# Kernel tuning notes

Measured on AMD Instinct MI355X. Metric: run time of the kernel, lower is better.

## Reference

```python
import jax, jax.numpy as jnp
import numpy as np

VOCAB, E, H, L = 32000, 512, 1024, 2
B, T = 64, 256


def _lstm_layer(x_seq, Wx, Wh, b):
    """x_seq: [T, B, in]. Gate order i,f,n,o stacked along last dim of Wx/Wh/b."""
    Bsz = x_seq.shape[1]
    h0 = jnp.zeros((Bsz, H), x_seq.dtype)
    c0 = jnp.zeros((Bsz, H), x_seq.dtype)

    def step(carry, x_t):
        h, c = carry
        g = x_t @ Wx + h @ Wh + b  # [B, 4H]
        i_t, f_t, n_t, o_t = jnp.split(g, 4, axis=-1)
        i_t = jax.nn.sigmoid(i_t)
        f_t = jax.nn.sigmoid(f_t)
        n_t = jnp.tanh(n_t)
        o_t = jax.nn.sigmoid(o_t)
        c_new = f_t * c + i_t * n_t
        h_new = o_t * jnp.tanh(c_new)
        return (h_new, c_new), h_new

    (h_n, c_n), ys = jax.lax.scan(step, (h0, c0), x_seq)
    return ys, h_n, c_n


def setup_inputs() -> dict:
    key = jax.random.key(0)
    ks = jax.random.split(key, 8)
    src = jax.random.randint(ks[0], (B, T), 0, VOCAB, dtype=jnp.int64 if jax.config.jax_enable_x64 else jnp.int32)
    lengths = jnp.sort(jax.random.randint(ks[1], (B,), T // 2, T + 1, dtype=jnp.int32))[::-1]
    lengths = lengths.at[0].set(T)  # guarantee max length == T (pad_packed_sequence output width)
    s = 0.05
    return {
        "src": src,
        "src_lengths": lengths,
        "embedding": jax.random.normal(ks[2], (VOCAB, E), jnp.float32) * s,
        "Wx0": jax.random.normal(ks[3], (E, 4 * H), jnp.float32) * s,
        "Wh0": jax.random.normal(ks[4], (H, 4 * H), jnp.float32) * s,
        "b0": jnp.zeros((4 * H,), jnp.float32),
        "Wx1": jax.random.normal(ks[5], (H, 4 * H), jnp.float32) * s,
        "Wh1": jax.random.normal(ks[6], (H, 4 * H), jnp.float32) * s,
        "b1": jnp.zeros((4 * H,), jnp.float32),
    }


def reference(src, src_lengths, embedding, Wx0, Wh0, b0, Wx1, Wh1, b1):
    # embedding lookup: [B, T, E]
    emb = embedding[src]
    x = jnp.transpose(emb, (1, 0, 2))  # [T, B, E]

    h_list, c_list = [], []
    for Wx, Wh, b in ((Wx0, Wh0, b0), (Wx1, Wh1, b1)):
        x, h_n, c_n = _lstm_layer(x, Wx, Wh, b)
        h_list.append(h_n)
        c_list.append(c_n)

    outputs = jnp.transpose(x, (1, 0, 2))  # [B, T, H]
    # pad_packed_sequence zeros out positions beyond each sequence length
    mask = (jnp.arange(T)[None, :] < src_lengths[:, None])[:, :, None]
    outputs = jnp.where(mask, outputs, jnp.zeros((), outputs.dtype))
    h_n = jnp.stack(h_list, axis=0)  # [L, B, H] (last-timestep states, as in CustomLSTM)
    c_n = jnp.stack(c_list, axis=0)
    return outputs, h_n, c_n
```

## Files before the change

### kernel.cpp

```cpp
#include <hip/hip_runtime.h>
#include <hip/hip_bf16.h>


typedef short bf16x8 __attribute__((ext_vector_type(8)));
typedef float f32x4 __attribute__((ext_vector_type(4)));

__device__ __forceinline__ float bf2f(ushort u) {
  union { unsigned int i; float f; } v; v.i = ((unsigned int)u) << 16; return v.f;
}
__device__ __forceinline__ ushort f2bf(float f) {
  union { float f; unsigned int i; } v; v.f = f;
  unsigned int r = v.i + 0x7fffu + ((v.i >> 16) & 1u);
  return (ushort)(r >> 16);
}

__global__ __launch_bounds__(256) void transpose_cvt(const float* __restrict__ W,
                                                     ushort* __restrict__ WT, int K) {
  __shared__ ushort t[64][65];
  int bn = blockIdx.x * 64;
  int bk = blockIdx.y * 64;
  for (int s = threadIdx.x; s < 4096; s += 256) {
    int kl = s >> 6, nl = s & 63;
    t[kl][nl] = f2bf(W[(size_t)(bk + kl) * 4096 + bn + nl]);
  }
  __syncthreads();
  for (int s = threadIdx.x; s < 4096; s += 256) {
    int nl = s >> 6, kl = s & 63;
    WT[(size_t)(bn + nl) * K + bk + kl] = t[kl][nl];
  }
}

__device__ __forceinline__ int swz(int row, int kElem) {
  int byte = row * 128 + kElem * 2;
  return byte ^ ((row & 7) << 4);
}

template <bool AF32>
__global__ __launch_bounds__(256) void gemm_xw(const void* __restrict__ Av,
                                               const int* __restrict__ gather, int tbase,
                                               const ushort* __restrict__ WT,
                                               const float* __restrict__ bias,
                                               ushort* __restrict__ G, int K) {
  int bx = blockIdx.x & 31;
  int by = blockIdx.x >> 5;
  int tid = threadIdx.x;
  int w = tid >> 6, l = tid & 63;
  int wr = w >> 1, wc = w & 1;
  int lr = l & 15, lk = (l >> 4) * 8;

  __shared__ alignas(16) char At[128 * 64 * 2];
  __shared__ alignas(16) char Bt[128 * 64 * 2];

  int srow = tid >> 3;
  int skof = (tid & 7) * 8;

  size_t aoff[4];
  const ushort* brow[4];
#pragma unroll
  for (int c2 = 0; c2 < 4; ++c2) {
    int m = by * 128 + c2 * 32 + srow;
    long idx = gather ? (long)gather[(m & 63) * 256 + tbase + (m >> 6)] : (long)m;
    aoff[c2] = (size_t)idx * K + skof;
    int n = bx * 128 + c2 * 32 + srow;
    brow[c2] = WT + (size_t)n * K + skof;
  }

  f32x4 zero = {0.f, 0.f, 0.f, 0.f};
  f32x4 acc[4][4];
#pragma unroll
  for (int i = 0; i < 4; ++i)
#pragma unroll
    for (int j = 0; j < 4; ++j) acc[i][j] = zero;

  for (int kc = 0; kc < K; kc += 64) {
    bf16x8 ar[4], br[4];
#pragma unroll
    for (int c2 = 0; c2 < 4; ++c2) {
      if (AF32) {
        const float* p = (const float*)Av + aoff[c2] + kc;
        f32x4 x0 = *(const f32x4*)p;
        f32x4 x1 = *(const f32x4*)(p + 4);
#pragma unroll
        for (int j = 0; j < 4; ++j) {
          ar[c2][j] = (short)f2bf(x0[j]);
          ar[c2][4 + j] = (short)f2bf(x1[j]);
        }
      } else {
        ar[c2] = *(const bf16x8*)((const ushort*)Av + aoff[c2] + kc);
      }
      br[c2] = *(const bf16x8*)(brow[c2] + kc);
    }
    __syncthreads();
#pragma unroll
    for (int c2 = 0; c2 < 4; ++c2) {
      *(bf16x8*)(At + swz(c2 * 32 + srow, skof)) = ar[c2];
      *(bf16x8*)(Bt + swz(c2 * 32 + srow, skof)) = br[c2];
    }
    __syncthreads();
#pragma unroll
    for (int ks = 0; ks < 2; ++ks) {
      bf16x8 af[4], bfr[4];
#pragma unroll
      for (int mt = 0; mt < 4; ++mt)
        af[mt] = *(const bf16x8*)(At + swz(wr * 64 + mt * 16 + lr, ks * 32 + lk));
#pragma unroll
      for (int nt = 0; nt < 4; ++nt)
        bfr[nt] = *(const bf16x8*)(Bt + swz(wc * 64 + nt * 16 + lr, ks * 32 + lk));
#pragma unroll
      for (int mt = 0; mt < 4; ++mt)
#pragma unroll
        for (int nt = 0; nt < 4; ++nt)
          acc[mt][nt] = __builtin_amdgcn_mfma_f32_16x16x32_bf16(af[mt], bfr[nt], acc[mt][nt], 0, 0, 0);
    }
  }

#pragma unroll
  for (int mt = 0; mt < 4; ++mt) {
#pragma unroll
    for (int nt = 0; nt < 4; ++nt) {
      int ncol = bx * 128 + wc * 64 + nt * 16 + lr;
      float bv = bias[ncol];
#pragma unroll
      for (int j = 0; j < 4; ++j) {
        int r = by * 128 + wr * 64 + mt * 16 + (l >> 4) * 4 + j;
        G[(size_t)r * 4096 + ncol] = f2bf(acc[mt][nt][j] + bv);
      }
    }
  }
}

template <bool OUTF32>
__global__ __launch_bounds__(64) void lstm_step(const ushort* __restrict__ hprev,
                                                ushort* __restrict__ hnext,
                                                float* __restrict__ cbuf,
                                                const ushort* __restrict__ WhT,
                                                const ushort* __restrict__ Gt,
                                                void* __restrict__ outp,
                                                long out_rstride,
                                                const int* __restrict__ lens,
                                                int t) {
  int bx = blockIdx.x & 63;
  int by = blockIdx.x >> 6;
  int l = threadIdx.x;
  int lr = l & 15, lk = (l >> 4) * 8;

  const ushort* arow = hprev + (by * 16 + lr) * 1024 + lk;
  const ushort* brow = WhT + (size_t)(bx * 16 + lr) * 1024 + lk;

  f32x4 zero = {0.f, 0.f, 0.f, 0.f};
  f32x4 acc[4];
  acc[0] = zero; acc[1] = zero; acc[2] = zero; acc[3] = zero;

#pragma unroll 8
  for (int ks = 0; ks < 32; ++ks) {
    bf16x8 a = *(const bf16x8*)(arow + ks * 32);
#pragma unroll
    for (int g = 0; g < 4; ++g) {
      bf16x8 b = *(const bf16x8*)(brow + (size_t)g * (1024 * 1024) + ks * 32);
      acc[g] = __builtin_amdgcn_mfma_f32_16x16x32_bf16(a, b, acc[g], 0, 0, 0);
    }
  }

  int ch = bx * 16 + lr;
#pragma unroll
  for (int j = 0; j < 4; ++j) {
    int rr = by * 16 + (l >> 4) * 4 + j;
    const ushort* grow = Gt + (size_t)rr * 4096 + ch;
    float gi = acc[0][j] + bf2f(grow[0]);
    float gf = acc[1][j] + bf2f(grow[1024]);
    float gn = acc[2][j] + bf2f(grow[2048]);
    float go = acc[3][j] + bf2f(grow[3072]);
    float i_ = 1.f / (1.f + expf(-gi));
    float f_ = 1.f / (1.f + expf(-gf));
    float n_ = tanhf(gn);
    float o_ = 1.f / (1.f + expf(-go));
    int ci = rr * 1024 + ch;
    float cn = f_ * cbuf[ci] + i_ * n_;
    cbuf[ci] = cn;
    float hv = o_ * tanhf(cn);
    hnext[ci] = f2bf(hv);
    if (OUTF32) {
      float ov = (t < lens[rr]) ? hv : 0.f;
      ((float*)outp)[(size_t)rr * out_rstride + ch] = ov;
    } else {
      ((ushort*)outp)[(size_t)rr * out_rstride + ch] = f2bf(hv);
    }
  }
}

__global__ __launch_bounds__(256) void init_hc(ushort* h, float* c) {
  int i = blockIdx.x * 256 + threadIdx.x;
  h[i] = 0;
  c[i] = 0.f;
}

__global__ __launch_bounds__(256) void write_states(const ushort* __restrict__ h,
                                                    const float* __restrict__ c,
                                                    float* __restrict__ oh,
                                                    float* __restrict__ oc) {
  int i = blockIdx.x * 256 + threadIdx.x;
  oh[i] = bf2f(h[i]);
  oc[i] = c[i];
}

extern "C" void kernel_launch(void* const* d_in, const int* in_sizes, int n_in,
                              void* d_out, int out_size, void* d_ws, size_t ws_size,
                              hipStream_t stream) {
  (void)in_sizes; (void)n_in; (void)out_size; (void)ws_size;
  const int* src    = (const int*)d_in[0];
  const int* lens   = (const int*)d_in[1];
  const float* emb  = (const float*)d_in[2];
  const float* Wx0  = (const float*)d_in[3];
  const float* Wh0  = (const float*)d_in[4];
  const float* b0   = (const float*)d_in[5];
  const float* Wx1  = (const float*)d_in[6];
  const float* Wh1  = (const float*)d_in[7];
  const float* b1   = (const float*)d_in[8];
  float* out = (float*)d_out;

  char* ws = (char*)d_ws;
  ushort* Wx0T = (ushort*)(ws + 0);
  ushort* Wh0T = (ushort*)(ws + 4194304);
  ushort* Wx1T = (ushort*)(ws + 12582912);
  ushort* Wh1T = (ushort*)(ws + 20971520);
  ushort* G    = (ushort*)(ws + 29360128);
  ushort* X1   = (ushort*)(ws + 62914560);
  ushort* hA   = (ushort*)(ws + 96468992);
  ushort* hB   = (ushort*)(ws + 96600064);
  float*  cbuf = (float*) (ws + 96731136);

  transpose_cvt<<<dim3(64, 8),  256, 0, stream>>>(Wx0, Wx0T, 512);
  transpose_cvt<<<dim3(64, 16), 256, 0, stream>>>(Wh0, Wh0T, 1024);
  transpose_cvt<<<dim3(64, 16), 256, 0, stream>>>(Wx1, Wx1T, 1024);
  transpose_cvt<<<dim3(64, 16), 256, 0, stream>>>(Wh1, Wh1T, 1024);

  init_hc<<<256, 256, 0, stream>>>(hA, cbuf);
  for (int c = 0; c < 4; ++c) {
    gemm_xw<true><<<1024, 256, 0, stream>>>(emb, src, c * 64, Wx0T, b0, G, 512);
    for (int tl = 0; tl < 64; ++tl) {
      int t = c * 64 + tl;
      const ushort* hp = (t & 1) ? hB : hA;
      ushort* hn = (t & 1) ? hA : hB;
      lstm_step<false><<<256, 64, 0, stream>>>(hp, hn, cbuf, Wh0T, G + (size_t)tl * 262144,
                                               X1 + (size_t)t * 65536, 1024, nullptr, t);
    }
  }
  write_states<<<256, 256, 0, stream>>>(hA, cbuf, out + 16777216, out + 16908288);

  init_hc<<<256, 256, 0, stream>>>(hA, cbuf);
  for (int c = 0; c < 4; ++c) {
    gemm_xw<false><<<1024, 256, 0, stream>>>(X1 + (size_t)c * 4194304, nullptr, 0, Wx1T, b1, G, 1024);
    for (int tl = 0; tl < 64; ++tl) {
      int t = c * 64 + tl;
      const ushort* hp = (t & 1) ? hB : hA;
      ushort* hn = (t & 1) ? hA : hB;
      lstm_step<true><<<256, 64, 0, stream>>>(hp, hn, cbuf, Wh1T, G + (size_t)tl * 262144,
                                              out + (size_t)t * 1024, 262144, lens, t);
    }
  }
  write_states<<<256, 256, 0, stream>>>(hA, cbuf, out + 16777216 + 65536, out + 16908288 + 65536);
}
```

Before: 6.882 ms.

## Replace per-timestep launches with persistent chunk kernel using grid barriers

```diff
diff --git a/kernel.cpp b/kernel.cpp
--- a/kernel.cpp
+++ b/kernel.cpp
@@ -129,69 +129,136 @@
   }
 }
 
-template <bool OUTF32>
-__global__ __launch_bounds__(64) void lstm_step(const ushort* __restrict__ hprev,
-                                                ushort* __restrict__ hnext,
-                                                float* __restrict__ cbuf,
-                                                const ushort* __restrict__ WhT,
-                                                const ushort* __restrict__ Gt,
-                                                void* __restrict__ outp,
-                                                long out_rstride,
-                                                const int* __restrict__ lens,
-                                                int t) {
-  int bx = blockIdx.x & 63;
-  int by = blockIdx.x >> 6;
-  int l = threadIdx.x;
-  int lr = l & 15, lk = (l >> 4) * 8;
-
-  const ushort* arow = hprev + (by * 16 + lr) * 1024 + lk;
-  const ushort* brow = WhT + (size_t)(bx * 16 + lr) * 1024 + lk;
-
-  f32x4 zero = {0.f, 0.f, 0.f, 0.f};
-  f32x4 acc[4];
-  acc[0] = zero; acc[1] = zero; acc[2] = zero; acc[3] = zero;
-
-#pragma unroll 8
-  for (int ks = 0; ks < 32; ++ks) {
-    bf16x8 a = *(const bf16x8*)(arow + ks * 32);
-#pragma unroll
-    for (int g = 0; g < 4; ++g) {
-      bf16x8 b = *(const bf16x8*)(brow + (size_t)g * (1024 * 1024) + ks * 32);
-      acc[g] = __builtin_amdgcn_mfma_f32_16x16x32_bf16(a, b, acc[g], 0, 0, 0);
-    }
-  }
-
-  int ch = bx * 16 + lr;
+template <int LAYER>
+__global__ __launch_bounds__(256) void lstm_chunk(
+    const ushort* __restrict__ WhT,
+    const ushort* __restrict__ G,
+    ushort* __restrict__ X1,
+    ushort* __restrict__ hA,
+    ushort* __restrict__ hB,
+    const ushort* __restrict__ hzero,
+    float* __restrict__ cbuf,
+    float* __restrict__ outF,
+    const int* __restrict__ lens,
+    int tbase,
+    int* __restrict__ cnt) {
+  const int bx = blockIdx.x;
+  const int tid = threadIdx.x;
+  const int w = tid >> 6;
+  const int l = tid & 63;
+  const int lr = l & 15;
+  const int lq = l >> 4;
+
+  __shared__ f32x4 red[4][4][4][64];
+
+  bf16x8 wreg[4][8];
+  {
+    const ushort* wb = WhT + (size_t)(bx * 16 + lr) * 1024 + w * 256 + lq * 8;
+#pragma unroll
+    for (int g = 0; g < 4; ++g)
+#pragma unroll
+      for (int kk = 0; kk < 8; ++kk)
+        wreg[g][kk] = *(const bf16x8*)(wb + (size_t)g * 1048576 + kk * 32);
+  }
+
+  const int ch = bx * 16 + lr;
+  const int rbase = w * 16 + lq * 4;
+  float c_[4];
+  int len_[4];
 #pragma unroll
   for (int j = 0; j < 4; ++j) {
-    int rr = by * 16 + (l >> 4) * 4 + j;
-    const ushort* grow = Gt + (size_t)rr * 4096 + ch;
-    float gi = acc[0][j] + bf2f(grow[0]);
-    float gf = acc[1][j] + bf2f(grow[1024]);
-    float gn = acc[2][j] + bf2f(grow[2048]);
-    float go = acc[3][j] + bf2f(grow[3072]);
-    float i_ = 1.f / (1.f + expf(-gi));
-    float f_ = 1.f / (1.f + expf(-gf));
-    float n_ = tanhf(gn);
-    float o_ = 1.f / (1.f + expf(-go));
-    int ci = rr * 1024 + ch;
-    float cn = f_ * cbuf[ci] + i_ * n_;
-    cbuf[ci] = cn;
-    float hv = o_ * tanhf(cn);
-    hnext[ci] = f2bf(hv);
-    if (OUTF32) {
-      float ov = (t < lens[rr]) ? hv : 0.f;
-      ((float*)outp)[(size_t)rr * out_rstride + ch] = ov;
+    c_[j] = cbuf[(rbase + j) * 1024 + ch];
+    len_[j] = (LAYER == 1) ? lens[rbase + j] : 0;
+  }
+
+  for (int s = 0; s < 64; ++s) {
+    const int t = tbase + s;
+    const ushort* hp;
+    ushort* hn;
+    if (LAYER == 0) {
+      hp = (t == 0) ? hzero : X1 + (size_t)(t - 1) * 65536;
+      hn = X1 + (size_t)t * 65536;
     } else {
-      ((ushort*)outp)[(size_t)rr * out_rstride + ch] = f2bf(hv);
-    }
-  }
-}
-
-__global__ __launch_bounds__(256) void init_hc(ushort* h, float* c) {
+      hp = (t & 1) ? hB : hA;
+      hn = (t & 1) ? hA : hB;
+    }
+
+    f32x4 acc[4][4];
+#pragma unroll
+    for (int m = 0; m < 4; ++m)
+#pragma unroll
+      for (int g = 0; g < 4; ++g)
+        acc[m][g] = (f32x4){0.f, 0.f, 0.f, 0.f};
+
+#pragma unroll
+    for (int kk = 0; kk < 8; ++kk) {
+      bf16x8 a[4];
+#pragma unroll
+      for (int m = 0; m < 4; ++m)
+        a[m] = *(const bf16x8*)(hp + (size_t)(m * 16 + lr) * 1024 + w * 256 + kk * 32 + lq * 8);
+#pragma unroll
+      for (int m = 0; m < 4; ++m)
+#pragma unroll
+        for (int g = 0; g < 4; ++g)
+          acc[m][g] = __builtin_amdgcn_mfma_f32_16x16x32_bf16(a[m], wreg[g][kk], acc[m][g], 0, 0, 0);
+    }
+
+#pragma unroll
+    for (int m = 0; m < 4; ++m)
+#pragma unroll
+      for (int g = 0; g < 4; ++g)
+        red[w][m][g][l] = acc[m][g];
+    __syncthreads();
+
+    f32x4 sg[4];
+#pragma unroll
+    for (int g = 0; g < 4; ++g)
+      sg[g] = red[0][w][g][l] + red[1][w][g][l] + red[2][w][g][l] + red[3][w][g][l];
+
+#pragma unroll
+    for (int j = 0; j < 4; ++j) {
+      const int rr = rbase + j;
+      const ushort* grow = G + ((size_t)(s * 64 + rr)) * 4096 + ch;
+      float gi = sg[0][j] + bf2f(grow[0]);
+      float gf = sg[1][j] + bf2f(grow[1024]);
+      float gn = sg[2][j] + bf2f(grow[2048]);
+      float go = sg[3][j] + bf2f(grow[3072]);
+      float i_ = 1.f / (1.f + expf(-gi));
+      float f_ = 1.f / (1.f + expf(-gf));
+      float n_ = tanhf(gn);
+      float o_ = 1.f / (1.f + expf(-go));
+      float cn = f_ * c_[j] + i_ * n_;
+      c_[j] = cn;
+      float hv = o_ * tanhf(cn);
+      hn[rr * 1024 + ch] = f2bf(hv);
+      if (LAYER == 1)
+        outF[(size_t)rr * 262144 + (size_t)t * 1024 + ch] = (t < len_[j]) ? hv : 0.f;
+    }
+
+    if (s != 63) {
+      __syncthreads();
+      if (tid == 0) {
+        __threadfence();
+        __hip_atomic_fetch_add(&cnt[s], 1, __ATOMIC_RELEASE, __HIP_MEMORY_SCOPE_AGENT);
+        int guard = 1 << 20;
+        while (__hip_atomic_load(&cnt[s], __ATOMIC_RELAXED, __HIP_MEMORY_SCOPE_AGENT) < 64 &&
+               --guard)
+          __builtin_amdgcn_s_sleep(2);
+      }
+      __syncthreads();
+      __threadfence();
+    }
+  }
+
+#pragma unroll
+  for (int j = 0; j < 4; ++j)
+    cbuf[(rbase + j) * 1024 + ch] = c_[j];
+}
+
+__global__ __launch_bounds__(256) void zero_mem(uint* __restrict__ p, int n) {
   int i = blockIdx.x * 256 + threadIdx.x;
-  h[i] = 0;
-  c[i] = 0.f;
+  int stride = gridDim.x * 256;
+  for (; i < n; i += stride) p[i] = 0u;
 }
 
 __global__ __launch_bounds__(256) void write_states(const ushort* __restrict__ h,
@@ -219,44 +286,41 @@
   float* out = (float*)d_out;
 
   char* ws = (char*)d_ws;
-  ushort* Wx0T = (ushort*)(ws + 0);
-  ushort* Wh0T = (ushort*)(ws + 4194304);
-  ushort* Wx1T = (ushort*)(ws + 12582912);
-  ushort* Wh1T = (ushort*)(ws + 20971520);
-  ushort* G    = (ushort*)(ws + 29360128);
-  ushort* X1   = (ushort*)(ws + 62914560);
-  ushort* hA   = (ushort*)(ws + 96468992);
-  ushort* hB   = (ushort*)(ws + 96600064);
-  float*  cbuf = (float*) (ws + 96731136);
+  ushort* Wx0T  = (ushort*)(ws + 0);
+  ushort* Wh0T  = (ushort*)(ws + 4194304);
+  ushort* Wx1T  = (ushort*)(ws + 12582912);
+  ushort* Wh1T  = (ushort*)(ws + 20971520);
+  ushort* G     = (ushort*)(ws + 29360128);
+  ushort* X1    = (ushort*)(ws + 62914560);
+  ushort* hA    = (ushort*)(ws + 96468992);
+  float*  cbuf  = (float*) (ws + 96600064);
+  ushort* hzero = (ushort*)(ws + 96862208);
+  int*    cnt   = (int*)   (ws + 96993280);
+  ushort* hB    = (ushort*)(ws + 96995328);
 
   transpose_cvt<<<dim3(64, 8),  256, 0, stream>>>(Wx0, Wx0T, 512);
   transpose_cvt<<<dim3(64, 16), 256, 0, stream>>>(Wh0, Wh0T, 1024);
   transpose_cvt<<<dim3(64, 16), 256, 0, stream>>>(Wx1, Wx1T, 1024);
   transpose_cvt<<<dim3(64, 16), 256, 0, stream>>>(Wh1, Wh1T, 1024);
 
-  init_hc<<<256, 256, 0, stream>>>(hA, cbuf);
+  zero_mem<<<128, 256, 0, stream>>>((uint*)hA, 526336 / 4);
+
   for (int c = 0; c < 4; ++c) {
     gemm_xw<true><<<1024, 256, 0, stream>>>(emb, src, c * 64, Wx0T, b0, G, 512);
-    for (int tl = 0; tl < 64; ++tl) {
-      int t = c * 64 + tl;
-      const ushort* hp = (t & 1) ? hB : hA;
-      ushort* hn = (t & 1) ? hA : hB;
-      lstm_step<false><<<256, 64, 0, stream>>>(hp, hn, cbuf, Wh0T, G + (size_t)tl * 262144,
-                                               X1 + (size_t)t * 65536, 1024, nullptr, t);
-    }
-  }
-  write_states<<<256, 256, 0, stream>>>(hA, cbuf, out + 16777216, out + 16908288);
-
-  init_hc<<<256, 256, 0, stream>>>(hA, cbuf);
+    lstm_chunk<0><<<64, 256, 0, stream>>>(Wh0T, G, X1, hA, hB, hzero, cbuf,
+                                          out, lens, c * 64, cnt + c * 64);
+  }
+  write_states<<<256, 256, 0, stream>>>(X1 + (size_t)255 * 65536, cbuf,
+                                        out + 16777216, out + 16908288);
+
+  zero_mem<<<128, 256, 0, stream>>>((uint*)hA, 393216 / 4);
+
   for (int c = 0; c < 4; ++c) {
-    gemm_xw<false><<<1024, 256, 0, stream>>>(X1 + (size_t)c * 4194304, nullptr, 0, Wx1T, b1, G, 1024);
-    for (int tl = 0; tl < 64; ++tl) {
-      int t = c * 64 + tl;
-      const ushort* hp = (t & 1) ? hB : hA;
-      ushort* hn = (t & 1) ? hA : hB;
-      lstm_step<true><<<256, 64, 0, stream>>>(hp, hn, cbuf, Wh1T, G + (size_t)tl * 262144,
-                                              out + (size_t)t * 1024, 262144, lens, t);
-    }
-  }
-  write_states<<<256, 256, 0, stream>>>(hA, cbuf, out + 16777216 + 65536, out + 16908288 + 65536);
-}
+    gemm_xw<false><<<1024, 256, 0, stream>>>(X1 + (size_t)c * 4194304, nullptr, 0,
+                                             Wx1T, b1, G, 1024);
+    lstm_chunk<1><<<64, 256, 0, stream>>>(Wh1T, G, X1, hA, hB, hzero, cbuf,
+                                          out, lens, c * 64, cnt + 256 + c * 64);
+  }
+  write_states<<<256, 256, 0, stream>>>(hA, cbuf,
+                                        out + 16777216 + 65536, out + 16908288 + 65536);
+}
```

After: 7.920 ms. +15.1%, slower.
